# Kernel tuning notes

Measured on AMD Instinct MI355X. Metric: run time of the kernel, lower is better.

Reference implementation:

```python
import jax, jax.numpy as jnp
import numpy as np

D_MODEL = 1024
N_HEADS = 16
HEAD_DIM = D_MODEL // N_HEADS
B, S = 4, 2048


def setup_inputs() -> dict:
    key = jax.random.key(0)
    ks = jax.random.split(key, 12)
    scale = 1.0 / np.sqrt(D_MODEL)
    inp = {
        "query": jax.random.normal(ks[0], (B, S, D_MODEL), dtype=jnp.float32),
        "key": jax.random.normal(ks[1], (B, S, D_MODEL), dtype=jnp.float32),
        "value": jax.random.normal(ks[2], (B, S, D_MODEL), dtype=jnp.float32),
        "mask": jnp.ones((B, 1, S), dtype=jnp.int32),
        "Wq": jax.random.normal(ks[3], (D_MODEL, D_MODEL), dtype=jnp.float32) * scale,
        "bq": jnp.zeros((D_MODEL,), dtype=jnp.float32),
        "Wk": jax.random.normal(ks[4], (D_MODEL, D_MODEL), dtype=jnp.float32) * scale,
        "bk": jnp.zeros((D_MODEL,), dtype=jnp.float32),
        "Wv": jax.random.normal(ks[5], (D_MODEL, D_MODEL), dtype=jnp.float32) * scale,
        "bv": jnp.zeros((D_MODEL,), dtype=jnp.float32),
        "Wo": jax.random.normal(ks[6], (D_MODEL, D_MODEL), dtype=jnp.float32) * scale,
        "bo": jnp.zeros((D_MODEL,), dtype=jnp.float32),
    }
    return inp


def reference(query, key, value, mask, Wq, bq, Wk, bk, Wv, bv, Wo, bo):
    bsz = query.shape[0]
    # Linear projections (torch nn.Linear: x @ W.T + b), split into heads -> [b, h, s, d]
    def proj(x, W, b):
        y = jnp.einsum("bse,de->bsd", x, W) + b
        return y.reshape(bsz, -1, N_HEADS, HEAD_DIM).transpose(0, 2, 1, 3)

    q = proj(query, Wq, bq)
    k = proj(key, Wk, bk)
    v = proj(value, Wv, bv)

    # NOTE: faithful to source — scale by 1/sqrt(d_model), not 1/sqrt(head_dim)
    scores = jnp.einsum("bhqd,bhkd->bhqk", q, k) / jnp.sqrt(jnp.asarray(D_MODEL, q.dtype))
    # mask [b, 1, s_k] -> unsqueeze(1) -> [b, 1, 1, s_k]; fill -inf where mask == 0
    m = mask[:, None, :, :]
    scores = jnp.where(m == 0, jnp.asarray(-jnp.inf, scores.dtype), scores)
    p_attn = jax.nn.softmax(scores, axis=-1)
    ctx = jnp.einsum("bhqk,bhkd->bhqd", p_attn, v)

    concat = ctx.transpose(0, 2, 1, 3).reshape(bsz, -1, D_MODEL)
    out = jnp.einsum("bse,de->bsd", concat, Wo) + bo
    return out
```

## Files before the change

### kernel.cpp

```cpp
#include <hip/hip_runtime.h>
#include <hip/hip_bf16.h>

typedef unsigned short u16;
typedef __attribute__((ext_vector_type(4))) short short4v;
typedef __attribute__((ext_vector_type(8))) short short8;
typedef __attribute__((ext_vector_type(4))) float float4v;
typedef __attribute__((ext_vector_type(16))) float f32x16;

__device__ __forceinline__ void async_copy16(const void* g, void* l) {
  __builtin_amdgcn_global_load_lds(
      (const __attribute__((address_space(1))) unsigned int*)g,
      (__attribute__((address_space(3))) unsigned int*)l,
      16, 0, 0);
}

__device__ __forceinline__ u16 f2bf(float f) {
  __hip_bfloat16 h = __float2bfloat16(f);
  return *reinterpret_cast<u16*>(&h);
}

__device__ __forceinline__ unsigned pack2(float a, float b) {
  return (unsigned)f2bf(a) | ((unsigned)f2bf(b) << 16);
}

__device__ __forceinline__ float exp2_fast(float x) {
  return __builtin_amdgcn_exp2f(x);
}

struct CArgs {
  const float* in[7];
  u16* out[7];
  int n[7];
};

__global__ void conv_bf16(CArgs a) {
  int t = blockIdx.y;
  int n = a.n[t];
  long i = ((long)blockIdx.x * blockDim.x + threadIdx.x) * 8;
  if (i >= n) return;
  const float4v* f = (const float4v*)(a.in[t] + i);
  float4v lo = f[0], hi = f[1];
  u16 o[8];
  o[0] = f2bf(lo.x); o[1] = f2bf(lo.y); o[2] = f2bf(lo.z); o[3] = f2bf(lo.w);
  o[4] = f2bf(hi.x); o[5] = f2bf(hi.y); o[6] = f2bf(hi.z); o[7] = f2bf(hi.w);
  *(short8*)(a.out[t] + i) = *(const short8*)o;
}

template <bool OUT_F32>
__device__ __forceinline__
void gemm_body(const u16* __restrict__ A, const u16* __restrict__ W,
               const float* __restrict__ bias, void* __restrict__ Cp,
               int M, int N, int K, int mode) {
  __shared__ __attribute__((aligned(16))) u16 As[128 * 32];
  __shared__ __attribute__((aligned(16))) u16 Ws[128 * 32];

  const int tid  = threadIdx.x;
  const int lane = tid & 63;
  const int wave = tid >> 6;
  const int ln15 = lane & 15;
  const int quad = lane >> 4;
  const int m0 = blockIdx.y * 128;
  const int n0 = blockIdx.x * 128;
  const int wm = (wave & 1) * 64;
  const int wn = (wave >> 1) * 64;

  float4v acc[4][4];
#pragma unroll
  for (int i = 0; i < 4; i++)
#pragma unroll
    for (int j = 0; j < 4; j++) acc[i][j] = (float4v)0.0f;

  for (int k0 = 0; k0 < K; k0 += 32) {
#pragma unroll
    for (int c = 0; c < 2; c++) {
      int e = (c * 256 + tid) * 8;
      int r = e >> 5, col = e & 31;
      async_copy16(A + (size_t)(m0 + r) * K + k0 + col, (void*)(As + e));
      async_copy16(W + (size_t)(n0 + r) * K + k0 + col, (void*)(Ws + e));
    }
    __syncthreads();

    short8 af[4], bfr[4];
#pragma unroll
    for (int i = 0; i < 4; i++)
      af[i] = *(const short8*)(As + (wm + i * 16 + ln15) * 32 + quad * 8);
#pragma unroll
    for (int j = 0; j < 4; j++)
      bfr[j] = *(const short8*)(Ws + (wn + j * 16 + ln15) * 32 + quad * 8);
#pragma unroll
    for (int i = 0; i < 4; i++)
#pragma unroll
      for (int j = 0; j < 4; j++)
        acc[i][j] = __builtin_amdgcn_mfma_f32_16x16x32_bf16(af[i], bfr[j], acc[i][j], 0, 0, 0);
    __syncthreads();
  }

#pragma unroll
  for (int j = 0; j < 4; j++) {
    int n = n0 + wn + j * 16 + ln15;
    float bval = bias[n];
#pragma unroll
    for (int i = 0; i < 4; i++) {
#pragma unroll
      for (int r = 0; r < 4; r++) {
        int m = m0 + wm + i * 16 + quad * 4 + r;
        float v = acc[i][j][r] + bval;
        size_t addr;
        if (mode == 0) {
          addr = (size_t)m * N + n;
        } else {
          int b = m >> 11, s = m & 2047;
          int h = n >> 6, dh = n & 63;
          if (mode == 1) addr = (((size_t)(b * 16 + h)) * 2048 + s) * 64 + dh;
          else           addr = (((size_t)(b * 16 + h)) * 64 + dh) * 2048 + s;
        }
        if (OUT_F32) ((float*)Cp)[addr] = v;
        else         ((u16*)Cp)[addr] = f2bf(v);
      }
    }
  }
}

template <bool OUT_F32>
__global__ __launch_bounds__(256, 3)
void gemm_bt(const u16* __restrict__ A, const u16* __restrict__ W,
             const float* __restrict__ bias, void* __restrict__ Cp,
             int M, int N, int K, int mode) {
  gemm_body<OUT_F32>(A, W, bias, Cp, M, N, K, mode);
}

struct G3 {
  const u16* A[3]; const u16* W[3]; const float* bias[3];
  void* C[3]; int mode[3];
};

__global__ __launch_bounds__(256, 3)
void gemm_qkv(G3 g) {
  const int z = blockIdx.z;
  gemm_body<false>(g.A[z], g.W[z], g.bias[z], g.C[z], 8192, 1024, 1024, g.mode[z]);
}

#define SWZ(c, r) ((c) ^ (((r) & 7) << 3))
__global__ __launch_bounds__(256, 4)
void attn(const u16* __restrict__ Q, const u16* __restrict__ K,
          const u16* __restrict__ Vt, const int* __restrict__ mask,
          u16* __restrict__ Ct) {
  __shared__ __attribute__((aligned(16))) u16 Ks[2][64 * 64];
  __shared__ __attribute__((aligned(16))) u16 Vs[2][64 * 64];

  const int tid  = threadIdx.x;
  const int lane = tid & 63;
  const int wave = tid >> 6;
  const int ln31 = lane & 31;
  const int hi   = lane >> 5;
  const int bh = blockIdx.y;
  const int b = bh >> 4, h = bh & 15;
  const int q0 = blockIdx.x * 128;
  const int qr0 = wave * 32;

  const u16* Qg = Q + ((size_t)bh * 2048 + q0 + qr0) * 64;
  const u16* Kg = K + (size_t)bh * 2048 * 64;
  const u16* Vg = Vt + (size_t)bh * 64 * 2048;
  const int* mg = mask + b * 2048;

  const float C2 = 0.04508422f;

  short8 qf[4];
#pragma unroll
  for (int m = 0; m < 4; m++)
    qf[m] = *(const short8*)(Qg + (size_t)ln31 * 64 + m * 16 + hi * 8);

#pragma unroll
  for (int c = 0; c < 2; c++) {
    int e = (c * 256 + tid) * 8;
    int r = e >> 6, col = e & 63;
    int sc = SWZ(col, r);
    *(short8*)(Ks[0] + r * 64 + sc) = *(const short8*)(Kg + (size_t)r * 64 + col);
    *(short8*)(Vs[0] + r * 64 + sc) = *(const short8*)(Vg + (size_t)r * 2048 + col);
  }

  f32x16 acc[2];
#pragma unroll
  for (int d = 0; d < 2; d++) acc[d] = (f32x16)0.0f;
  float lrow = 0.0f;

  for (int t = 0; t < 32; t++) {
    const int buf = t & 1;
    __syncthreads();

    short8 kreg[2], vreg[2];
    const bool havenext = (t + 1) < 32;
    if (havenext) {
      int kt2 = (t + 1) * 64;
#pragma unroll
      for (int c = 0; c < 2; c++) {
        int e = (c * 256 + tid) * 8;
        int r = e >> 6, col = e & 63;
        kreg[c] = *(const short8*)(Kg + (size_t)(kt2 + r) * 64 + col);
        vreg[c] = *(const short8*)(Vg + (size_t)r * 2048 + kt2 + col);
      }
    }

    unsigned bw[2][2][4];
#pragma unroll
    for (int kb = 0; kb < 2; kb++) {
      f32x16 s = (f32x16)0.0f;
      __builtin_amdgcn_s_setprio(1);
#pragma unroll
      for (int m = 0; m < 4; m++) {
        const int krow = kb * 32 + ln31;
        short8 kf = *(const short8*)(Ks[buf] + krow * 64 + SWZ(m * 16 + hi * 8, krow));
        s = __builtin_amdgcn_mfma_f32_32x32x16_bf16(kf, qf[m], s, 0, 0, 0);
      }
      __builtin_amdgcn_s_setprio(0);
      unsigned w[8];
#pragma unroll
      for (int g = 0; g < 4; g++) {
        int4 m4 = *(const int4*)(mg + t * 64 + kb * 32 + g * 8 + hi * 4);
        float mb0 = (m4.x == 0) ? -1.5e30f : 0.0f;
        float mb1 = (m4.y == 0) ? -1.5e30f : 0.0f;
        float mb2 = (m4.z == 0) ? -1.5e30f : 0.0f;
        float mb3 = (m4.w == 0) ? -1.5e30f : 0.0f;
        float p0 = exp2_fast(fmaf(s[4 * g + 0], C2, mb0));
        float p1 = exp2_fast(fmaf(s[4 * g + 1], C2, mb1));
        float p2 = exp2_fast(fmaf(s[4 * g + 2], C2, mb2));
        float p3 = exp2_fast(fmaf(s[4 * g + 3], C2, mb3));
        lrow += (p0 + p1) + (p2 + p3);
        w[2 * g]     = pack2(p0, p1);
        w[2 * g + 1] = pack2(p2, p3);
      }
#pragma unroll
      for (int c = 0; c < 2; c++) {
        auto r0 = __builtin_amdgcn_permlane32_swap(w[c], w[2 + c], false, false);
        bw[kb][0][c]     = r0[0];
        bw[kb][0][2 + c] = r0[1];
        auto r1 = __builtin_amdgcn_permlane32_swap(w[4 + c], w[6 + c], false, false);
        bw[kb][1][c]     = r1[0];
        bw[kb][1][2 + c] = r1[1];
      }
    }

    if (havenext) {
#pragma unroll
      for (int c = 0; c < 2; c++) {
        int e = (c * 256 + tid) * 8;
        int r = e >> 6, col = e & 63;
        int sc = SWZ(col, r);
        *(short8*)(Ks[buf ^ 1] + r * 64 + sc) = kreg[c];
        *(short8*)(Vs[buf ^ 1] + r * 64 + sc) = vreg[c];
      }
    }

    __builtin_amdgcn_s_setprio(1);
#pragma unroll
    for (int d = 0; d < 2; d++) {
#pragma unroll
      for (int kb = 0; kb < 2; kb++) {
#pragma unroll
        for (int mp = 0; mp < 2; mp++) {
          const int vrow = d * 32 + ln31;
          short8 vf = *(const short8*)(Vs[buf] + vrow * 64 +
                                       SWZ(kb * 32 + mp * 16 + hi * 8, vrow));
          union { unsigned w4[4]; short8 s8; } u;
          u.w4[0] = bw[kb][mp][0]; u.w4[1] = bw[kb][mp][1];
          u.w4[2] = bw[kb][mp][2]; u.w4[3] = bw[kb][mp][3];
          acc[d] = __builtin_amdgcn_mfma_f32_32x32x16_bf16(vf, u.s8, acc[d], 0, 0, 0);
        }
      }
    }
    __builtin_amdgcn_s_setprio(0);
  }

  float l = lrow + __shfl_xor(lrow, 32);
  float inv = 1.0f / l;
  const int s = q0 + qr0 + ln31;
  u16* base = Ct + ((size_t)(b * 2048 + s)) * 1024 + h * 64 + hi * 4;
#pragma unroll
  for (int d = 0; d < 2; d++) {
#pragma unroll
    for (int g = 0; g < 4; g++) {
      u16 o[4];
      o[0] = f2bf(acc[d][4 * g + 0] * inv);
      o[1] = f2bf(acc[d][4 * g + 1] * inv);
      o[2] = f2bf(acc[d][4 * g + 2] * inv);
      o[3] = f2bf(acc[d][4 * g + 3] * inv);
      *(short4v*)(base + d * 32 + g * 8) = *(const short4v*)o;
    }
  }
}


extern "C" void kernel_launch(void* const* d_in, const int* in_sizes, int n_in,
                              void* d_out, int out_size, void* d_ws, size_t ws_size,
                              hipStream_t stream) {
  int iq, ik, iv, im, iWq, ibq, iWk, ibk, iWv, ibv, iWo, ibo;
  if (in_sizes[0] == 8388608) {
    iq = 0; ik = 1; iv = 2; im = 3;
    iWq = 4; ibq = 5; iWk = 6; ibk = 7; iWv = 8; ibv = 9; iWo = 10; ibo = 11;
  } else {
    iWk = 0; iWo = 1; iWq = 2; iWv = 3;
    ibk = 4; ibo = 5; ibq = 6; ibv = 7;
    ik = 8; im = 9; iq = 10; iv = 11;
  }
  const float* query = (const float*)d_in[iq];
  const float* key   = (const float*)d_in[ik];
  const float* value = (const float*)d_in[iv];
  const int*   mask  = (const int*)d_in[im];
  const float* Wq = (const float*)d_in[iWq];
  const float* bq = (const float*)d_in[ibq];
  const float* Wk = (const float*)d_in[iWk];
  const float* bk = (const float*)d_in[ibk];
  const float* Wv = (const float*)d_in[iWv];
  const float* bv = (const float*)d_in[ibv];
  const float* Wo = (const float*)d_in[iWo];
  const float* bo = (const float*)d_in[ibo];

  const long U  = 8388608;
  const long Wn = 1048576;
  u16* ws = (u16*)d_ws;
  u16* cq   = ws;
  u16* ck   = cq + U;
  u16* cv   = ck + U;
  u16* cWq  = cv + U;
  u16* cWk  = cWq + Wn;
  u16* cWv  = cWk + Wn;
  u16* cWo  = cWv + Wn;
  u16* qws  = cWo + Wn;
  u16* kws  = qws + U;
  u16* cws  = ck;

  const size_t need_batched = (size_t)(7 * U + 4 * Wn) * sizeof(u16);
  const bool batched = ws_size >= need_batched;
  u16* vtws = batched ? (kws + U) : cq;

  dim3 blk(256);

  CArgs ca;
  ca.in[0] = query; ca.out[0] = cq;  ca.n[0] = (int)U;
  ca.in[1] = key;   ca.out[1] = ck;  ca.n[1] = (int)U;
  ca.in[2] = value; ca.out[2] = cv;  ca.n[2] = (int)U;
  ca.in[3] = Wq;    ca.out[3] = cWq; ca.n[3] = (int)Wn;
  ca.in[4] = Wk;    ca.out[4] = cWk; ca.n[4] = (int)Wn;
  ca.in[5] = Wv;    ca.out[5] = cWv; ca.n[5] = (int)Wn;
  ca.in[6] = Wo;    ca.out[6] = cWo; ca.n[6] = (int)Wn;
  conv_bf16<<<dim3(4096, 7), blk, 0, stream>>>(ca);

  dim3 gproj(8, 64);
  if (batched) {
    G3 g3;
    g3.A[0] = cq; g3.W[0] = cWq; g3.bias[0] = bq; g3.C[0] = qws;  g3.mode[0] = 1;
    g3.A[1] = ck; g3.W[1] = cWk; g3.bias[1] = bk; g3.C[1] = kws;  g3.mode[1] = 1;
    g3.A[2] = cv; g3.W[2] = cWv; g3.bias[2] = bv; g3.C[2] = vtws; g3.mode[2] = 2;
    gemm_qkv<<<dim3(8, 64, 3), blk, 0, stream>>>(g3);
  } else {
    gemm_bt<false><<<gproj, blk, 0, stream>>>(cq, cWq, bq, qws, 8192, 1024, 1024, 1);
    gemm_bt<false><<<gproj, blk, 0, stream>>>(ck, cWk, bk, kws, 8192, 1024, 1024, 1);
    gemm_bt<false><<<gproj, blk, 0, stream>>>(cv, cWv, bv, vtws, 8192, 1024, 1024, 2);
  }
  attn<<<dim3(16, 64), blk, 0, stream>>>(qws, kws, vtws, mask, cws);
  gemm_bt<true><<<gproj, blk, 0, stream>>>(cws, cWo, bo, d_out, 8192, 1024, 1024, 0);
}
```

Before: 429.2 us.

## Use async global-to-LDS copies for attention K/V tiles and swizzle GEMM block order

The attention kernel's K/V double-buffer prefetch now uses global_load_lds direct copies instead of loading into registers and storing to LDS. The swizzle moves to the source address, so each thread writes linearly into LDS. This removes the register staging and the explicit LDS stores, freeing VGPRs and VALU issue slots. The GEMM also remaps block indices so consecutive workgroups are spread across the N tiles, likely for better cache or XCD locality. The risk is that the async copies lack an explicit vmcnt wait before the barrier, so correctness depends on the barrier or compiler inserting one.

```diff
diff --git a/kernel.cpp b/kernel.cpp
--- a/kernel.cpp
+++ b/kernel.cpp
@@ -59,8 +59,20 @@
   const int wave = tid >> 6;
   const int ln15 = lane & 15;
   const int quad = lane >> 4;
-  const int m0 = blockIdx.y * 128;
-  const int n0 = blockIdx.x * 128;
+
+  int bx = blockIdx.x, by = blockIdx.y;
+  {
+    const int nwg = gridDim.x * gridDim.y;
+    if (gridDim.x == 8 && (nwg & 7) == 0) {
+      const int per = nwg >> 3;
+      const int bid = by * 8 + bx;
+      const int nlin = (bid & 7) * per + (bid >> 3);
+      bx = nlin & 7;
+      by = nlin >> 3;
+    }
+  }
+  const int m0 = by * 128;
+  const int n0 = bx * 128;
   const int wm = (wave & 1) * 64;
   const int wn = (wave >> 1) * 64;
 
@@ -165,6 +177,7 @@
 
   const float C2 = 0.04508422f;
 
+
   short8 qf[4];
 #pragma unroll
   for (int m = 0; m < 4; m++)
@@ -174,9 +187,9 @@
   for (int c = 0; c < 2; c++) {
     int e = (c * 256 + tid) * 8;
     int r = e >> 6, col = e & 63;
-    int sc = SWZ(col, r);
-    *(short8*)(Ks[0] + r * 64 + sc) = *(const short8*)(Kg + (size_t)r * 64 + col);
-    *(short8*)(Vs[0] + r * 64 + sc) = *(const short8*)(Vg + (size_t)r * 2048 + col);
+    int scol = SWZ(col, r);
+    async_copy16(Kg + (size_t)r * 64 + scol, (void*)(Ks[0] + e));
+    async_copy16(Vg + (size_t)r * 2048 + scol, (void*)(Vs[0] + e));
   }
 
   f32x16 acc[2];
@@ -188,16 +201,15 @@
     const int buf = t & 1;
     __syncthreads();
 
-    short8 kreg[2], vreg[2];
-    const bool havenext = (t + 1) < 32;
-    if (havenext) {
-      int kt2 = (t + 1) * 64;
+    if ((t + 1) < 32) {
+      const int kt2 = (t + 1) * 64;
 #pragma unroll
       for (int c = 0; c < 2; c++) {
         int e = (c * 256 + tid) * 8;
         int r = e >> 6, col = e & 63;
-        kreg[c] = *(const short8*)(Kg + (size_t)(kt2 + r) * 64 + col);
-        vreg[c] = *(const short8*)(Vg + (size_t)r * 2048 + kt2 + col);
+        int scol = SWZ(col, r);
+        async_copy16(Kg + (size_t)(kt2 + r) * 64 + scol, (void*)(Ks[buf ^ 1] + e));
+        async_copy16(Vg + (size_t)r * 2048 + kt2 + scol, (void*)(Vs[buf ^ 1] + e));
       }
     }
 
@@ -240,17 +252,6 @@
       }
     }
 
-    if (havenext) {
-#pragma unroll
-      for (int c = 0; c < 2; c++) {
-        int e = (c * 256 + tid) * 8;
-        int r = e >> 6, col = e & 63;
-        int sc = SWZ(col, r);
-        *(short8*)(Ks[buf ^ 1] + r * 64 + sc) = kreg[c];
-        *(short8*)(Vs[buf ^ 1] + r * 64 + sc) = vreg[c];
-      }
-    }
-
     __builtin_amdgcn_s_setprio(1);
 #pragma unroll
     for (int d = 0; d < 2; d++) {
```

New measurement: 390.7 us. -9.0%, faster.
